# Kernel optimization log

Hardware: AMD Instinct MI355X
Metric: run time of the kernel (lower is better)

## Reference

```python
import jax, jax.numpy as jnp
import numpy as np

B, G, N, D = 2, 2, 2048, 512
H, DH = 8, 64
DI = H * DH  # dim_inner = 512


def rmsnorm(x, gamma):
    # x: [b, g, n, d]; original normalizes over feature dim (F.normalize, eps=1e-12)
    norm = jnp.linalg.norm(x, axis=-1, keepdims=True)
    normed = x / jnp.maximum(norm, 1e-12)
    return normed * jnp.sqrt(jnp.asarray(x.shape[-1], x.dtype)) * gamma[None, :, None, :]


def setup_inputs() -> dict:
    key = jax.random.key(0)
    ks = jax.random.split(key, 8)
    x = jax.random.normal(ks[0], (B, G, N, D), dtype=jnp.float32)
    mask = jax.random.randint(ks[1], (B, N), 0, 2) > 0
    gamma_q = jnp.ones((G, D), dtype=jnp.float32)
    gamma_c = jnp.ones((G, D), dtype=jnp.float32)
    s = 0.02
    wq = jax.random.normal(ks[2], (G, DI, D), dtype=jnp.float32) * s
    wkv = jax.random.normal(ks[3], (G, 2 * DI, D), dtype=jnp.float32) * s
    wout = jax.random.normal(ks[4], (G, D, DI), dtype=jnp.float32) * s
    null_kv = jax.random.normal(ks[5], (2, G, H, 1, DH), dtype=jnp.float32)
    return {"x": x, "mask": mask, "gamma_q": gamma_q, "gamma_c": gamma_c,
            "wq": wq, "wkv": wkv, "wout": wout, "null_kv": null_kv}


def reference(x, mask, gamma_q, gamma_c, wq, wkv, wout, null_kv):
    b, g, n, d = x.shape
    # prenorm (context = x, so both norms applied to same input)
    xq = rmsnorm(x, gamma_q)
    xc = rmsnorm(x, gamma_c)
    # grouped 1x1 conv projections == per-group matmuls
    q = jnp.einsum('bgnd,ged->bgne', xq, wq)                 # [b,g,n,DI]
    kv = jnp.einsum('bgnd,ged->bgne', xc, wkv)               # [b,g,n,2*DI]
    k, v = jnp.split(kv, 2, axis=-1)
    def split_heads(t):
        return t.reshape(b, g, n, H, DH).transpose(0, 1, 3, 2, 4)  # [b,g,h,n,dh]
    q, k, v = map(split_heads, (q, k, v))
    # null kv: concat along sequence dim
    nk = jnp.broadcast_to(null_kv[0][None], (b, g, H, 1, DH))
    nv = jnp.broadcast_to(null_kv[1][None], (b, g, H, 1, DH))
    k = jnp.concatenate([nk, k], axis=-2)                    # [b,g,h,n+1,dh]
    v = jnp.concatenate([nv, v], axis=-2)
    # attention
    scale = DH ** -0.5
    scores = jnp.einsum('bghid,bghjd->bghij', q, k) * scale  # [b,g,h,n,n+1]
    m = jnp.concatenate([jnp.ones((b, 1), dtype=bool), mask], axis=-1)  # pad True for null kv
    scores = jnp.where(m[:, None, None, None, :], scores, jnp.asarray(-1e30, scores.dtype))
    attn = jax.nn.softmax(scores, axis=-1)
    out = jnp.einsum('bghij,bghjd->bghid', attn, v)          # [b,g,h,n,dh]
    out = out.transpose(0, 1, 3, 2, 4).reshape(b, g, n, DI)  # merge heads
    out = jnp.einsum('bgne,gde->bgnd', out, wout)
    return out
```

## Files before the change

### kernel.cpp

```cpp
#include <hip/hip_runtime.h>
#include <stdint.h>

typedef unsigned short u16;
typedef __attribute__((ext_vector_type(8))) short  bf16x8;
typedef __attribute__((ext_vector_type(8))) u16    u16x8;
typedef __attribute__((ext_vector_type(4))) u16    u16x4;
typedef __attribute__((ext_vector_type(4))) float  f32x4;
typedef __attribute__((ext_vector_type(2))) unsigned u32x2;

#define SEQ 2048
#define DIM 512
#define NH  8
#define NBG 4
#define QSCALE 0.18033688011112042f

__device__ __forceinline__ float bf2f(u16 u) { return __uint_as_float(((unsigned)u) << 16); }
__device__ __forceinline__ u16 f2bf(float f) {
  unsigned u = __float_as_uint(f);
  return (u16)((u + 0x7FFFu + ((u >> 16) & 1u)) >> 16);
}
__device__ __forceinline__ float h2f(u16 u) { return (float)__builtin_bit_cast(_Float16, u); }
__device__ __forceinline__ u16 f2h(float f) { return __builtin_bit_cast(unsigned short, (_Float16)f); }

__device__ __forceinline__ float ex2(float x) {
#if __has_builtin(__builtin_amdgcn_exp2f)
  return __builtin_amdgcn_exp2f(x);
#else
  return exp2f(x);
#endif
}

__device__ __forceinline__ void gload_lds16(const void* g, void* l) {
#if __has_builtin(__builtin_amdgcn_global_load_lds)
  __builtin_amdgcn_global_load_lds((__attribute__((address_space(1))) void*)g,
                                   (__attribute__((address_space(3))) void*)l, 16, 0, 0);
#else
  *(u16x8*)l = *(const u16x8*)g;
#endif
}

__device__ __forceinline__ int float_mode(const void* gq) {
  unsigned w0 = *(const unsigned*)gq;
  return (w0 == 0x3F800000u) ? 1 : ((w0 == 0x3C003C00u) ? 2 : 0);
}
__device__ __forceinline__ int mask_mode(const void* maskp) {
  const unsigned* mw = (const unsigned*)maskp;
  bool all01 = true, lowhit = false, f32ish = true;
#pragma unroll
  for (int i = 0; i < 64; i++) {
    unsigned v = mw[i];
    all01 = all01 && (v <= 1u);
    lowhit = lowhit || ((v & 0xFFFFu) == 0x3F80u) || ((v & 0xFFFFu) == 0x3C00u);
    f32ish = f32ish && (v == 0u || v == 0x3F800000u);
  }
  return all01 ? 0 : (lowhit ? 1 : (f32ish ? 2 : 3));
}
__device__ __forceinline__ bool mask_at(const void* m, int idx, int mode) {
  if (mode == 0) return ((const int*)m)[idx] != 0;
  if (mode == 1) return ((const u16*)m)[idx] != 0;
  if (mode == 2) return ((const float*)m)[idx] != 0.f;
  return ((const unsigned char*)m)[idx] != 0;
}
__device__ __forceinline__ float ldf(const void* p, int i, int mode) {
  if (mode == 1) return ((const float*)p)[i];
  if (mode == 2) return h2f(((const u16*)p)[i]);
  return bf2f(((const u16*)p)[i]);
}

__global__ __launch_bounds__(256) void pre_kernel(
    const void* __restrict__ x, const void* __restrict__ gq, const void* __restrict__ gc,
    const void* __restrict__ wq, const void* __restrict__ wkv, const void* __restrict__ wout,
    const void* __restrict__ nkv,
    u16* __restrict__ wqb, u16* __restrict__ wkvb, u16* __restrict__ woutb, u16* __restrict__ nkvb,
    u16* __restrict__ xn)
{
  const int NWQ = 2*512*512, NWKV = 2*1024*512, NWOUT = 2*512*512;
  int mode = float_mode(gq);
  if (blockIdx.x < 1025) {
    int loc = (blockIdx.x * 256 + threadIdx.x) * 8;
    const void* s; u16* d; int fold = 0; const void* gam = nullptr; int gbase = 0; float ex = 1.f;
    if (loc < NWQ) { s = wq; d = wqb; fold = 1; gam = gq; gbase = ((loc >> 18) << 9) | (loc & 511); ex = QSCALE; }
    else { loc -= NWQ;
      if (loc < NWKV) { s = wkv; d = wkvb; fold = 1; gam = gc; gbase = ((loc >> 19) << 9) | (loc & 511); }
      else { loc -= NWKV;
        if (loc < NWOUT) { s = wout; d = woutb; }
        else { loc -= NWOUT; if (loc < 2048) { s = nkv; d = nkvb; } else return; } } }
    u16x8 o;
#pragma unroll
    for (int j = 0; j < 8; j++) {
      float v = ldf(s, loc + j, mode) * ex;
      if (fold) v *= ldf(gam, gbase + j, mode);
      o[j] = f2bf(v);
    }
    *(u16x8*)(d + loc) = o;
    return;
  }
  int row  = (blockIdx.x - 1025) * 4 + (threadIdx.x >> 6);
  int lane = threadIdx.x & 63;
  float f[8];
  if (mode == 1) {
    const float* xr = (const float*)x + (size_t)row * DIM + lane * 8;
    f32x4 a = *(const f32x4*)xr, b2 = *(const f32x4*)(xr + 4);
#pragma unroll
    for (int i = 0; i < 4; i++) { f[i] = a[i]; f[i + 4] = b2[i]; }
  } else if (mode == 2) {
    u16x8 v = *(const u16x8*)((const u16*)x + (size_t)row * DIM + lane * 8);
#pragma unroll
    for (int i = 0; i < 8; i++) f[i] = h2f(v[i]);
  } else {
    u16x8 v = *(const u16x8*)((const u16*)x + (size_t)row * DIM + lane * 8);
#pragma unroll
    for (int i = 0; i < 8; i++) f[i] = bf2f(v[i]);
  }
  float ss = 0.f;
#pragma unroll
  for (int i = 0; i < 8; i++) ss += f[i] * f[i];
#pragma unroll
  for (int off = 32; off; off >>= 1) ss += __shfl_xor(ss, off);
  float scale = 22.62741699796952f / fmaxf(sqrtf(ss), 1e-12f);
  u16x8 o;
#pragma unroll
  for (int i = 0; i < 8; i++) o[i] = f2bf(f[i] * scale);
  *(u16x8*)(xn + (size_t)row * DIM + lane * 8) = o;
}

__global__ __launch_bounds__(256, 4) void gemm_qkv(
    const u16* __restrict__ A, const u16* __restrict__ wqb, const u16* __restrict__ wkvb,
    u16* __restrict__ qb, u16* __restrict__ kb, u16* __restrict__ vtb)
{
  __shared__ u16 As[128 * 64], Bs[64 * 64];
  int bg = blockIdx.z, g = bg & 1;
  int y = blockIdx.y;
  const u16* Bw; u16* C; u16* C2; int Ncols, splitcol, bn0;
  if (y < 8) { Bw = wqb;  C = qb; C2 = nullptr; Ncols = 512;  splitcol = 1 << 30; bn0 = y * 64; }
  else       { Bw = wkvb; C = kb; C2 = vtb;     Ncols = 1024; splitcol = 512;     bn0 = (y - 8) * 64; }
  const int M = SEQ, K = DIM, ldc = 512;
  int bm0 = blockIdx.x * 128;
  int tid = threadIdx.x, w = tid >> 6, l = tid & 63;
  int li = l & 15, lg = l >> 4;
  int wr = w >> 1, wc = w & 1;
  const u16* Ab = A + (size_t)bg * M * K;
  const u16* Bb = Bw + (size_t)g * Ncols * K;
  f32x4 acc[4][2];
#pragma unroll
  for (int m = 0; m < 4; m++)
#pragma unroll
    for (int n = 0; n < 2; n++) acc[m][n] = (f32x4){0.f, 0.f, 0.f, 0.f};
  for (int kt = 0; kt < K; kt += 64) {
#pragma unroll
    for (int i = 0; i < 4; i++) {
      int ch = i * 256 + tid;
      gload_lds16(Ab + (size_t)(bm0 + (ch >> 3)) * K + kt + ((ch & 7) << 3), &As[ch * 8]);
    }
#pragma unroll
    for (int i = 0; i < 2; i++) {
      int ch = i * 256 + tid;
      gload_lds16(Bb + (size_t)(bn0 + (ch >> 3)) * K + kt + ((ch & 7) << 3), &Bs[ch * 8]);
    }
    __syncthreads();
#pragma unroll
    for (int kk = 0; kk < 2; kk++) {
      bf16x8 a[4], b[2];
#pragma unroll
      for (int m = 0; m < 4; m++) a[m] = *(const bf16x8*)&As[(wr * 64 + m * 16 + li) * 64 + kk * 32 + lg * 8];
#pragma unroll
      for (int n = 0; n < 2; n++) b[n] = *(const bf16x8*)&Bs[(wc * 32 + n * 16 + li) * 64 + kk * 32 + lg * 8];
      __builtin_amdgcn_s_setprio(1);
#pragma unroll
      for (int m = 0; m < 4; m++)
#pragma unroll
        for (int n = 0; n < 2; n++)
          acc[m][n] = __builtin_amdgcn_mfma_f32_16x16x32_bf16(a[m], b[n], acc[m][n], 0, 0, 0);
      __builtin_amdgcn_s_setprio(0);
    }
    __syncthreads();
  }
#pragma unroll
  for (int m = 0; m < 4; m++) {
#pragma unroll
    for (int n = 0; n < 2; n++) {
      int row = bm0 + wr * 64 + m * 16 + lg * 4;
      int col = bn0 + wc * 32 + n * 16 + li;
      if (col < splitcol) {
        u16* cp = C + (size_t)bg * M * ldc + (size_t)row * ldc + col;
#pragma unroll
        for (int r = 0; r < 4; r++) cp[(size_t)r * ldc] = f2bf(acc[m][n][r]);
      } else {
        u16x4 pk;
#pragma unroll
        for (int r = 0; r < 4; r++) pk[r] = f2bf(acc[m][n][r]);
        *(u16x4*)&C2[(size_t)bg * 512 * M + (size_t)(col - 512) * M + row] = pk;
      }
    }
  }
}

__global__ __launch_bounds__(256, 4) void gemm_out(
    const u16* __restrict__ A, const u16* __restrict__ Bw,
    void* __restrict__ Cout, const void* __restrict__ gq0)
{
  __shared__ u16 As[128 * 64], Bs[64 * 64];
  const int M = SEQ, K = DIM, ldc = 512;
  int bg = blockIdx.z, g = bg & 1;
  int bm0 = blockIdx.x * 128, bn0 = blockIdx.y * 64;
  int tid = threadIdx.x, w = tid >> 6, l = tid & 63;
  int li = l & 15, lg = l >> 4;
  int wr = w >> 1, wc = w & 1;
  const u16* Ab = A + (size_t)bg * M * K;
  const u16* Bb = Bw + (size_t)g * 512 * K;
  f32x4 acc[4][2];
#pragma unroll
  for (int m = 0; m < 4; m++)
#pragma unroll
    for (int n = 0; n < 2; n++) acc[m][n] = (f32x4){0.f, 0.f, 0.f, 0.f};
  for (int kt = 0; kt < K; kt += 64) {
#pragma unroll
    for (int i = 0; i < 4; i++) {
      int ch = i * 256 + tid;
      gload_lds16(Ab + (size_t)(bm0 + (ch >> 3)) * K + kt + ((ch & 7) << 3), &As[ch * 8]);
    }
#pragma unroll
    for (int i = 0; i < 2; i++) {
      int ch = i * 256 + tid;
      gload_lds16(Bb + (size_t)(bn0 + (ch >> 3)) * K + kt + ((ch & 7) << 3), &Bs[ch * 8]);
    }
    __syncthreads();
#pragma unroll
    for (int kk = 0; kk < 2; kk++) {
      bf16x8 a[4], b[2];
#pragma unroll
      for (int m = 0; m < 4; m++) a[m] = *(const bf16x8*)&As[(wr * 64 + m * 16 + li) * 64 + kk * 32 + lg * 8];
#pragma unroll
      for (int n = 0; n < 2; n++) b[n] = *(const bf16x8*)&Bs[(wc * 32 + n * 16 + li) * 64 + kk * 32 + lg * 8];
      __builtin_amdgcn_s_setprio(1);
#pragma unroll
      for (int m = 0; m < 4; m++)
#pragma unroll
        for (int n = 0; n < 2; n++)
          acc[m][n] = __builtin_amdgcn_mfma_f32_16x16x32_bf16(a[m], b[n], acc[m][n], 0, 0, 0);
      __builtin_amdgcn_s_setprio(0);
    }
    __syncthreads();
  }
  int mode = float_mode(gq0);
#pragma unroll
  for (int m = 0; m < 4; m++) {
#pragma unroll
    for (int n = 0; n < 2; n++) {
      int row = bm0 + wr * 64 + m * 16 + lg * 4;
      int col = bn0 + wc * 32 + n * 16 + li;
      if (mode == 1) {
        float* cp = (float*)Cout + (size_t)bg * M * ldc + (size_t)row * ldc + col;
#pragma unroll
        for (int r = 0; r < 4; r++) cp[(size_t)r * ldc] = acc[m][n][r];
      } else if (mode == 2) {
        u16* cp = (u16*)Cout + (size_t)bg * M * ldc + (size_t)row * ldc + col;
#pragma unroll
        for (int r = 0; r < 4; r++) cp[(size_t)r * ldc] = f2h(acc[m][n][r]);
      } else {
        u16* cp = (u16*)Cout + (size_t)bg * M * ldc + (size_t)row * ldc + col;
#pragma unroll
        for (int r = 0; r < 4; r++) cp[(size_t)r * ldc] = f2bf(acc[m][n][r]);
      }
    }
  }
}

__global__ __launch_bounds__(256, 2) void attn_kernel(
    const u16* __restrict__ q, const u16* __restrict__ k, const u16* __restrict__ vt,
    const u16* __restrict__ nkv, const void* __restrict__ maskp, u16* __restrict__ ao)
{
  __shared__ __align__(16) u16 Kb[2][64 * 64];
  __shared__ __align__(16) u16 Vb[2][64 * 64];
  __shared__ __align__(16) u16 Ps[4][2][16 * 72];
  __shared__ __align__(4)  u16 mpk[SEQ];
  const int bid = blockIdx.x;
  const int h = bid & 7, bg = (bid >> 3) & 3, ib = bid >> 5;
  const int b = bg >> 1, g = bg & 1;
  const int tid = threadIdx.x, w = tid >> 6, l = tid & 63;
  const int li = l & 15, lg = l >> 4;
  const int i0 = ib * 128 + w * 32;

  auto stage = [&](int t, int buf) {
    int jb = t * 64;
#pragma unroll
    for (int p = 0; p < 2; p++) {
      int idx = p * 256 + tid;
      int j = idx >> 3, G = idx & 7;
      int c = (G ^ (j & 7)) << 3;
      gload_lds16(k + ((size_t)bg * SEQ + jb + j) * DIM + h * 64 + c, &Kb[buf][idx * 8]);
    }
#pragma unroll
    for (int p = 0; p < 2; p++) {
      int idx = p * 256 + tid;
      int d = idx >> 3, G = idx & 7;
      int c = (G ^ (d & 7)) << 3;
      gload_lds16(vt + ((size_t)bg * DIM + h * 64 + d) * SEQ + jb + c, &Vb[buf][idx * 8]);
    }
  };

  stage(0, 0);
  {
    const int smode = mask_mode(maskp);
#pragma unroll
    for (int i = 0; i < SEQ / 256; i++)
      mpk[i * 256 + tid] = mask_at(maskp, b * SEQ + i * 256 + tid, smode) ? 0xFFFFu : 0u;
  }

  bf16x8 qf[2][2];
#pragma unroll
  for (int rg = 0; rg < 2; rg++)
#pragma unroll
    for (int kk = 0; kk < 2; kk++)
      qf[rg][kk] = *(const bf16x8*)&q[((size_t)bg * SEQ + i0 + rg * 16 + li) * DIM + h * 64 + kk * 32 + lg * 8];

  bf16x8 ones;
#pragma unroll
  for (int r = 0; r < 8; r++) ones[r] = (short)0x3F80;

  const u16* nk = nkv + ((size_t)g * NH + h) * 64;
  const u16* nv = nkv + ((size_t)(2 + g) * NH + h) * 64;
  f32x4 oacc[2][4], lacc[2];
#pragma unroll
  for (int rg = 0; rg < 2; rg++) {
    float s = 0.f;
#pragma unroll
    for (int kk = 0; kk < 2; kk++)
#pragma unroll
      for (int r = 0; r < 8; r++)
        s += bf2f((u16)qf[rg][kk][r]) * bf2f(nk[kk * 32 + lg * 8 + r]);
    s += __shfl_xor(s, 16); s += __shfl_xor(s, 32);
    float pn = ex2(s);
    lacc[rg] = (f32x4){pn, pn, pn, pn};
#pragma unroll
    for (int dm = 0; dm < 4; dm++) {
      f32x4 o;
#pragma unroll
      for (int r = 0; r < 4; r++) o[r] = pn * bf2f(nv[dm * 16 + lg * 4 + r]);
      oacc[rg][dm] = o;
    }
  }
  __syncthreads();

  const int NT = SEQ / 64;
  for (int t = 0; t < NT; t++) {
    int cur = t & 1;
    if (t + 1 < NT) stage(t + 1, cur ^ 1);

    bf16x8 kf[4][2];
#pragma unroll
    for (int jm = 0; jm < 4; jm++)
#pragma unroll
      for (int kk = 0; kk < 2; kk++) {
        int gsw = ((kk * 4 + lg) ^ (li & 7)) << 3;
        kf[jm][kk] = *(const bf16x8*)&Kb[cur][(jm * 16 + li) * 64 + gsw];
      }

    f32x4 s4[2][4];
    __builtin_amdgcn_s_setprio(1);
#pragma unroll
    for (int rg = 0; rg < 2; rg++)
#pragma unroll
      for (int jm = 0; jm < 4; jm++) {
        f32x4 z = {0.f, 0.f, 0.f, 0.f};
        z = __builtin_amdgcn_mfma_f32_16x16x32_bf16(kf[jm][0], qf[rg][0], z, 0, 0, 0);
        z = __builtin_amdgcn_mfma_f32_16x16x32_bf16(kf[jm][1], qf[rg][1], z, 0, 0, 0);
        s4[rg][jm] = z;
      }
    __builtin_amdgcn_s_setprio(0);

    int jb = t * 64;
#pragma unroll
    for (int rg = 0; rg < 2; rg++) {
      u16* pb = &Ps[w][rg][0];
#pragma unroll
      for (int jm = 0; jm < 4; jm++) {
        unsigned u0 = __float_as_uint(ex2(s4[rg][jm][0]));
        unsigned u1 = __float_as_uint(ex2(s4[rg][jm][1]));
        unsigned u2 = __float_as_uint(ex2(s4[rg][jm][2]));
        unsigned u3 = __float_as_uint(ex2(s4[rg][jm][3]));
        unsigned mm01 = *(const unsigned*)&mpk[jb + jm * 16 + lg * 4];
        unsigned mm23 = *(const unsigned*)&mpk[jb + jm * 16 + lg * 4 + 2];
        unsigned w01 = __builtin_amdgcn_perm(u1, u0, 0x07060302u) & mm01;
        unsigned w23 = __builtin_amdgcn_perm(u3, u2, 0x07060302u) & mm23;
        *(u32x2*)&pb[li * 72 + jm * 16 + lg * 4] = (u32x2){w01, w23};
      }
    }

    bf16x8 vf[4][2];
#pragma unroll
    for (int jm = 0; jm < 4; jm++)
#pragma unroll
      for (int kk = 0; kk < 2; kk++) {
        int gsw = ((kk * 4 + lg) ^ (li & 7)) << 3;
        vf[jm][kk] = *(const bf16x8*)&Vb[cur][(jm * 16 + li) * 64 + gsw];
      }
#pragma unroll
    for (int rg = 0; rg < 2; rg++) {
      const u16* pb = &Ps[w][rg][0];
      bf16x8 pf0 = *(const bf16x8*)&pb[li * 72 + lg * 8];
      bf16x8 pf1 = *(const bf16x8*)&pb[li * 72 + 32 + lg * 8];
      __builtin_amdgcn_s_setprio(1);
      lacc[rg] = __builtin_amdgcn_mfma_f32_16x16x32_bf16(ones, pf0, lacc[rg], 0, 0, 0);
      lacc[rg] = __builtin_amdgcn_mfma_f32_16x16x32_bf16(ones, pf1, lacc[rg], 0, 0, 0);
#pragma unroll
      for (int dm = 0; dm < 4; dm++) {
        oacc[rg][dm] = __builtin_amdgcn_mfma_f32_16x16x32_bf16(vf[dm][0], pf0, oacc[rg][dm], 0, 0, 0);
        oacc[rg][dm] = __builtin_amdgcn_mfma_f32_16x16x32_bf16(vf[dm][1], pf1, oacc[rg][dm], 0, 0, 0);
      }
      __builtin_amdgcn_s_setprio(0);
    }
    __syncthreads();
  }
#pragma unroll
  for (int rg = 0; rg < 2; rg++) {
    float inv = 1.f / lacc[rg][0];
#pragma unroll
    for (int dm = 0; dm < 4; dm++) {
      u16x4 o;
#pragma unroll
      for (int r = 0; r < 4; r++) o[r] = f2bf(oacc[rg][dm][r] * inv);
      *(u16x4*)&ao[((size_t)bg * SEQ + i0 + rg * 16 + li) * DIM + h * 64 + dm * 16 + lg * 4] = o;
    }
  }
}

extern "C" void kernel_launch(void* const* d_in, const int* in_sizes, int n_in,
                              void* d_out, int out_size, void* d_ws, size_t ws_size,
                              hipStream_t stream) {
  const void* x    = d_in[0];
  const void* msk  = d_in[1];
  const void* gq   = d_in[2];
  const void* gc   = d_in[3];
  const void* wq   = d_in[4];
  const void* wkv  = d_in[5];
  const void* wout = d_in[6];
  const void* nkv  = d_in[7];

  u16* base = (u16*)d_ws;
  const size_t SLOT = (size_t)NBG * SEQ * DIM;
  u16* xn = base + 0 * SLOT;
  u16* ao = base + 0 * SLOT;
  u16* qb = base + 1 * SLOT;
  u16* kb = base + 2 * SLOT;
  u16* vt = base + 3 * SLOT;
  u16* wreg = base + 4 * SLOT;
  const int NWQ = 2 * 512 * 512, NWKV = 2 * 1024 * 512, NWOUT = 2 * 512 * 512;
  u16* wqb   = wreg;
  u16* wkvb  = wreg + NWQ;
  u16* woutb = wreg + NWQ + NWKV;
  u16* nkvb  = wreg + NWQ + NWKV + NWOUT;

  hipLaunchKernelGGL(pre_kernel, dim3(3073), dim3(256), 0, stream,
                     x, gq, gc, wq, wkv, wout, nkv, wqb, wkvb, woutb, nkvb, xn);
  hipLaunchKernelGGL(gemm_qkv, dim3(16, 24, NBG), dim3(256), 0, stream,
                     xn, wqb, wkvb, qb, kb, vt);
  hipLaunchKernelGGL(attn_kernel, dim3(512), dim3(256), 0, stream,
                     qb, kb, vt, nkvb, msk, ao);
  hipLaunchKernelGGL(gemm_out, dim3(16, 8, NBG), dim3(256), 0, stream,
                     ao, woutb, d_out, gq);
}
```

Before: 104.2 us.

## Compact unmasked keys via prefix scan to skip masked attention tiles

Adds a prefix-sum over the key mask in the pre kernel, computing for each position its compacted index and the count of valid keys per batch. The K/V projection epilogue scatters only unmasked rows into a packed K and transposed V layout. The attention kernel then loops only over ceil(valid/64) tiles and masks just the tail, removing the per-tile mask loads and the work on masked keys (about half the keys for a random mask). It also reuses one P buffer per wave and loads V fragments inside the PV loop, trading scattered, uncoalesced epilogue stores for less attention work.

```diff
diff --git a/kernel.cpp b/kernel.cpp
--- a/kernel.cpp
+++ b/kernel.cpp
@@ -6,6 +6,7 @@
 typedef __attribute__((ext_vector_type(8))) u16    u16x8;
 typedef __attribute__((ext_vector_type(4))) u16    u16x4;
 typedef __attribute__((ext_vector_type(4))) float  f32x4;
+typedef __attribute__((ext_vector_type(4))) int    i32x4;
 typedef __attribute__((ext_vector_type(2))) unsigned u32x2;
 
 #define SEQ 2048
@@ -70,11 +71,35 @@
 __global__ __launch_bounds__(256) void pre_kernel(
     const void* __restrict__ x, const void* __restrict__ gq, const void* __restrict__ gc,
     const void* __restrict__ wq, const void* __restrict__ wkv, const void* __restrict__ wout,
-    const void* __restrict__ nkv,
+    const void* __restrict__ nkv, const void* __restrict__ maskp,
     u16* __restrict__ wqb, u16* __restrict__ wkvb, u16* __restrict__ woutb, u16* __restrict__ nkvb,
-    u16* __restrict__ xn)
+    u16* __restrict__ xn, int* __restrict__ np, int* __restrict__ nv)
 {
   const int NWQ = 2*512*512, NWKV = 2*1024*512, NWOUT = 2*512*512;
+  if (blockIdx.x >= 3073) {
+    __shared__ int sc[2][256];
+    int b = blockIdx.x - 3073;
+    int t = threadIdx.x;
+    const int smode = mask_mode(maskp);
+    int base = t * 8;
+    int loc[8]; int c = 0;
+#pragma unroll
+    for (int i = 0; i < 8; i++) { loc[i] = mask_at(maskp, b * SEQ + base + i, smode) ? 1 : 0; c += loc[i]; }
+    sc[0][t] = c;
+    int src = 0, v = c;
+    for (int off = 1; off < 256; off <<= 1) {
+      __syncthreads();
+      int add = (t >= off) ? sc[src][t - off] : 0;
+      v += add;
+      sc[src ^ 1][t] = v;
+      src ^= 1;
+    }
+    int run = v - c;
+#pragma unroll
+    for (int i = 0; i < 8; i++) { np[b * SEQ + base + i] = loc[i] ? run : -1; run += loc[i]; }
+    if (t == 255) nv[b] = v;
+    return;
+  }
   int mode = float_mode(gq);
   if (blockIdx.x < 1025) {
     int loc = (blockIdx.x * 256 + threadIdx.x) * 8;
@@ -126,14 +151,15 @@
 
 __global__ __launch_bounds__(256, 4) void gemm_qkv(
     const u16* __restrict__ A, const u16* __restrict__ wqb, const u16* __restrict__ wkvb,
-    u16* __restrict__ qb, u16* __restrict__ kb, u16* __restrict__ vtb)
+    u16* __restrict__ qb, u16* __restrict__ kb, u16* __restrict__ vtb,
+    const int* __restrict__ np)
 {
   __shared__ u16 As[128 * 64], Bs[64 * 64];
   int bg = blockIdx.z, g = bg & 1;
   int y = blockIdx.y;
-  const u16* Bw; u16* C; u16* C2; int Ncols, splitcol, bn0;
-  if (y < 8) { Bw = wqb;  C = qb; C2 = nullptr; Ncols = 512;  splitcol = 1 << 30; bn0 = y * 64; }
-  else       { Bw = wkvb; C = kb; C2 = vtb;     Ncols = 1024; splitcol = 512;     bn0 = (y - 8) * 64; }
+  const u16* Bw; int Ncols, bn0, isq;
+  if (y < 8) { Bw = wqb;  Ncols = 512;  bn0 = y * 64;       isq = 1; }
+  else       { Bw = wkvb; Ncols = 1024; bn0 = (y - 8) * 64; isq = 0; }
   const int M = SEQ, K = DIM, ldc = 512;
   int bm0 = blockIdx.x * 128;
   int tid = threadIdx.x, w = tid >> 6, l = tid & 63;
@@ -175,21 +201,35 @@
     }
     __syncthreads();
   }
-#pragma unroll
-  for (int m = 0; m < 4; m++) {
-#pragma unroll
-    for (int n = 0; n < 2; n++) {
+  if (isq) {
+#pragma unroll
+    for (int m = 0; m < 4; m++) {
+#pragma unroll
+      for (int n = 0; n < 2; n++) {
+        int row = bm0 + wr * 64 + m * 16 + lg * 4;
+        int col = bn0 + wc * 32 + n * 16 + li;
+        u16* cp = qb + (size_t)bg * M * ldc + (size_t)row * ldc + col;
+#pragma unroll
+        for (int r = 0; r < 4; r++) cp[(size_t)r * ldc] = f2bf(acc[m][n][r]);
+      }
+    }
+  } else {
+    const int* npb = np + (bg >> 1) * SEQ;
+#pragma unroll
+    for (int m = 0; m < 4; m++) {
       int row = bm0 + wr * 64 + m * 16 + lg * 4;
-      int col = bn0 + wc * 32 + n * 16 + li;
-      if (col < splitcol) {
-        u16* cp = C + (size_t)bg * M * ldc + (size_t)row * ldc + col;
-#pragma unroll
-        for (int r = 0; r < 4; r++) cp[(size_t)r * ldc] = f2bf(acc[m][n][r]);
-      } else {
-        u16x4 pk;
-#pragma unroll
-        for (int r = 0; r < 4; r++) pk[r] = f2bf(acc[m][n][r]);
-        *(u16x4*)&C2[(size_t)bg * 512 * M + (size_t)(col - 512) * M + row] = pk;
+      i32x4 nr4 = *(const i32x4*)&npb[row];
+#pragma unroll
+      for (int n = 0; n < 2; n++) {
+        int col = bn0 + wc * 32 + n * 16 + li;
+#pragma unroll
+        for (int r = 0; r < 4; r++) {
+          int nr = nr4[r];
+          if (nr >= 0) {
+            if (col < 512) kb[(size_t)bg * M * ldc + (size_t)nr * ldc + col] = f2bf(acc[m][n][r]);
+            else           vtb[(size_t)bg * 512 * M + (size_t)(col - 512) * M + nr] = f2bf(acc[m][n][r]);
+          }
+        }
       }
     }
   }
@@ -268,44 +308,39 @@
 
 __global__ __launch_bounds__(256, 2) void attn_kernel(
     const u16* __restrict__ q, const u16* __restrict__ k, const u16* __restrict__ vt,
-    const u16* __restrict__ nkv, const void* __restrict__ maskp, u16* __restrict__ ao)
+    const u16* __restrict__ nkv, const int* __restrict__ nv, u16* __restrict__ ao)
 {
   __shared__ __align__(16) u16 Kb[2][64 * 64];
   __shared__ __align__(16) u16 Vb[2][64 * 64];
-  __shared__ __align__(16) u16 Ps[4][2][16 * 72];
-  __shared__ __align__(4)  u16 mpk[SEQ];
+  __shared__ __align__(16) u16 Ps[4][16 * 72];
   const int bid = blockIdx.x;
   const int h = bid & 7, bg = (bid >> 3) & 3, ib = bid >> 5;
-  const int b = bg >> 1, g = bg & 1;
+  const int g = bg & 1;
   const int tid = threadIdx.x, w = tid >> 6, l = tid & 63;
   const int li = l & 15, lg = l >> 4;
   const int i0 = ib * 128 + w * 32;
+  const int nvb = nv[bg >> 1];
+  const int NT = (nvb + 63) >> 6;
 
   auto stage = [&](int t, int buf) {
     int jb = t * 64;
 #pragma unroll
     for (int p = 0; p < 2; p++) {
       int idx = p * 256 + tid;
-      int j = idx >> 3, G = idx & 7;
-      int c = (G ^ (j & 7)) << 3;
-      gload_lds16(k + ((size_t)bg * SEQ + jb + j) * DIM + h * 64 + c, &Kb[buf][idx * 8]);
+      int r = idx >> 3, G = idx & 7;
+      int c = (G ^ (r & 7)) << 3;
+      gload_lds16(k + ((size_t)bg * SEQ + jb + r) * DIM + h * 64 + c, &Kb[buf][idx * 8]);
     }
 #pragma unroll
     for (int p = 0; p < 2; p++) {
       int idx = p * 256 + tid;
-      int d = idx >> 3, G = idx & 7;
-      int c = (G ^ (d & 7)) << 3;
-      gload_lds16(vt + ((size_t)bg * DIM + h * 64 + d) * SEQ + jb + c, &Vb[buf][idx * 8]);
+      int r = idx >> 3, G = idx & 7;
+      int c = (G ^ (r & 7)) << 3;
+      gload_lds16(vt + ((size_t)bg * DIM + h * 64 + r) * SEQ + jb + c, &Vb[buf][idx * 8]);
     }
   };
 
-  stage(0, 0);
-  {
-    const int smode = mask_mode(maskp);
-#pragma unroll
-    for (int i = 0; i < SEQ / 256; i++)
-      mpk[i * 256 + tid] = mask_at(maskp, b * SEQ + i * 256 + tid, smode) ? 0xFFFFu : 0u;
-  }
+  if (NT > 0) stage(0, 0);
 
   bf16x8 qf[2][2];
 #pragma unroll
@@ -319,7 +354,7 @@
   for (int r = 0; r < 8; r++) ones[r] = (short)0x3F80;
 
   const u16* nk = nkv + ((size_t)g * NH + h) * 64;
-  const u16* nv = nkv + ((size_t)(2 + g) * NH + h) * 64;
+  const u16* nvp = nkv + ((size_t)(2 + g) * NH + h) * 64;
   f32x4 oacc[2][4], lacc[2];
 #pragma unroll
   for (int rg = 0; rg < 2; rg++) {
@@ -336,16 +371,16 @@
     for (int dm = 0; dm < 4; dm++) {
       f32x4 o;
 #pragma unroll
-      for (int r = 0; r < 4; r++) o[r] = pn * bf2f(nv[dm * 16 + lg * 4 + r]);
+      for (int r = 0; r < 4; r++) o[r] = pn * bf2f(nvp[dm * 16 + lg * 4 + r]);
       oacc[rg][dm] = o;
     }
   }
   __syncthreads();
 
-  const int NT = SEQ / 64;
   for (int t = 0; t < NT; t++) {
     int cur = t & 1;
     if (t + 1 < NT) stage(t + 1, cur ^ 1);
+    const bool tail = (t == NT - 1);
 
     bf16x8 kf[4][2];
 #pragma unroll
@@ -372,32 +407,23 @@
     int jb = t * 64;
 #pragma unroll
     for (int rg = 0; rg < 2; rg++) {
-      u16* pb = &Ps[w][rg][0];
+      u16* pb = &Ps[w][0];
 #pragma unroll
       for (int jm = 0; jm < 4; jm++) {
         unsigned u0 = __float_as_uint(ex2(s4[rg][jm][0]));
         unsigned u1 = __float_as_uint(ex2(s4[rg][jm][1]));
         unsigned u2 = __float_as_uint(ex2(s4[rg][jm][2]));
         unsigned u3 = __float_as_uint(ex2(s4[rg][jm][3]));
-        unsigned mm01 = *(const unsigned*)&mpk[jb + jm * 16 + lg * 4];
-        unsigned mm23 = *(const unsigned*)&mpk[jb + jm * 16 + lg * 4 + 2];
-        unsigned w01 = __builtin_amdgcn_perm(u1, u0, 0x07060302u) & mm01;
-        unsigned w23 = __builtin_amdgcn_perm(u3, u2, 0x07060302u) & mm23;
-        *(u32x2*)&pb[li * 72 + jm * 16 + lg * 4] = (u32x2){w01, w23};
-      }
-    }
-
-    bf16x8 vf[4][2];
-#pragma unroll
-    for (int jm = 0; jm < 4; jm++)
-#pragma unroll
-      for (int kk = 0; kk < 2; kk++) {
-        int gsw = ((kk * 4 + lg) ^ (li & 7)) << 3;
-        vf[jm][kk] = *(const bf16x8*)&Vb[cur][(jm * 16 + li) * 64 + gsw];
-      }
-#pragma unroll
-    for (int rg = 0; rg < 2; rg++) {
-      const u16* pb = &Ps[w][rg][0];
+        unsigned w01 = __builtin_amdgcn_perm(u1, u0, 0x07060302u);
+        unsigned w23 = __builtin_amdgcn_perm(u3, u2, 0x07060302u);
+        if (tail) {
+          int e0 = jb + jm * 16 + lg * 4;
+          unsigned t01 = (e0 + 0 < nvb ? 0x0000FFFFu : 0u) | (e0 + 1 < nvb ? 0xFFFF0000u : 0u);
+          unsigned t23 = (e0 + 2 < nvb ? 0x0000FFFFu : 0u) | (e0 + 3 < nvb ? 0xFFFF0000u : 0u);
+          w01 &= t01; w23 &= t23;
+        }
+        *(u32x2*)&Ps[w][li * 72 + jm * 16 + lg * 4] = (u32x2){w01, w23};
+      }
       bf16x8 pf0 = *(const bf16x8*)&pb[li * 72 + lg * 8];
       bf16x8 pf1 = *(const bf16x8*)&pb[li * 72 + 32 + lg * 8];
       __builtin_amdgcn_s_setprio(1);
@@ -405,13 +431,18 @@
       lacc[rg] = __builtin_amdgcn_mfma_f32_16x16x32_bf16(ones, pf1, lacc[rg], 0, 0, 0);
 #pragma unroll
       for (int dm = 0; dm < 4; dm++) {
-        oacc[rg][dm] = __builtin_amdgcn_mfma_f32_16x16x32_bf16(vf[dm][0], pf0, oacc[rg][dm], 0, 0, 0);
-        oacc[rg][dm] = __builtin_amdgcn_mfma_f32_16x16x32_bf16(vf[dm][1], pf1, oacc[rg][dm], 0, 0, 0);
+        int gsw0 = ((0 * 4 + lg) ^ (li & 7)) << 3;
+        int gsw1 = ((1 * 4 + lg) ^ (li & 7)) << 3;
+        bf16x8 vf0 = *(const bf16x8*)&Vb[cur][(dm * 16 + li) * 64 + gsw0];
+        bf16x8 vf1 = *(const bf16x8*)&Vb[cur][(dm * 16 + li) * 64 + gsw1];
+        oacc[rg][dm] = __builtin_amdgcn_mfma_f32_16x16x32_bf16(vf0, pf0, oacc[rg][dm], 0, 0, 0);
+        oacc[rg][dm] = __builtin_amdgcn_mfma_f32_16x16x32_bf16(vf1, pf1, oacc[rg][dm], 0, 0, 0);
       }
       __builtin_amdgcn_s_setprio(0);
     }
     __syncthreads();
   }
+
 #pragma unroll
   for (int rg = 0; rg < 2; rg++) {
     float inv = 1.f / lacc[rg][0];
@@ -450,13 +481,16 @@
   u16* wkvb  = wreg + NWQ;
   u16* woutb = wreg + NWQ + NWKV;
   u16* nkvb  = wreg + NWQ + NWKV + NWOUT;
-
-  hipLaunchKernelGGL(pre_kernel, dim3(3073), dim3(256), 0, stream,
-                     x, gq, gc, wq, wkv, wout, nkv, wqb, wkvb, woutb, nkvb, xn);
+  int* np    = (int*)(nkvb + 2048);
+  int* nv    = np + 2 * SEQ;
+
+  hipLaunchKernelGGL(pre_kernel, dim3(3075), dim3(256), 0, stream,
+                     x, gq, gc, wq, wkv, wout, nkv, msk,
+                     wqb, wkvb, woutb, nkvb, xn, np, nv);
   hipLaunchKernelGGL(gemm_qkv, dim3(16, 24, NBG), dim3(256), 0, stream,
-                     xn, wqb, wkvb, qb, kb, vt);
+                     xn, wqb, wkvb, qb, kb, vt, np);
   hipLaunchKernelGGL(attn_kernel, dim3(512), dim3(256), 0, stream,
-                     qb, kb, vt, nkvb, msk, ao);
+                     qb, kb, vt, nkvb, nv, ao);
   hipLaunchKernelGGL(gemm_out, dim3(16, 8, NBG), dim3(256), 0, stream,
                      ao, woutb, d_out, gq);
 }
```

Result: faster. 84.68 us (-18.7%).
